# Kernel optimization log

Measured on AMD Instinct MI355X. Metric: run time of the kernel, lower is better.

Reference implementation:

```python
import jax, jax.numpy as jnp
import numpy as np

H, D = 4, 32          # heads, per-head dim (= hidden_channels)
HD = H * D            # concat width fed between layers
L = 2                 # num HGT layers
OUT = 128             # final output dim
SCALE = 1.0 / np.sqrt(D)


def _seg_softmax(score, seg, n):
    # segment softmax over incoming edges per destination node, per head
    mx = jax.ops.segment_max(score, seg, num_segments=n)
    ex = jnp.exp(score - mx[seg])
    den = jax.ops.segment_sum(ex, seg, num_segments=n)
    return ex / den[seg]


def _hgt_side(q_dst, k_src, v_src, src, dst, a_rel, m_rel, p_rel, n_dst):
    # k/v: [N_src,H,D]; a_rel,m_rel: [H,D,D]; p_rel: [H]
    k_t = jnp.einsum('ehd,hdf->ehf', k_src[src], a_rel)          # [E,H,D]
    score = (q_dst[dst] * k_t).sum(-1) * p_rel * SCALE           # [E,H]
    alpha = _seg_softmax(score, dst, n_dst)                      # [E,H]
    v_t = jnp.einsum('ehd,hdf->ehf', v_src[src], m_rel)          # [E,H,D]
    return jax.ops.segment_sum(alpha[..., None] * v_t, dst, num_segments=n_dst)


def _forward(x_m, x_g, W_in_m, b_in_m, W_in_g, b_in_g,
             Wk_m, bk_m, Wq_m, bq_m, Wv_m, bv_m,
             Wk_g, bk_g, Wq_g, bq_g, Wv_g, bv_g,
             a_mg, m_mg, p_mg, a_gm, m_gm, p_gm,
             Wa_m, ba_m, Wa_g, ba_g, skip_m, skip_g,
             W_out_m, b_out_m, W_out_g, b_out_g,
             edge_mg_src, edge_mg_dst, edge_gm_src, edge_gm_dst):
    Nm, Ng = x_m.shape[0], x_g.shape[0]
    # per-node-type input projection
    h_m = x_m @ W_in_m + b_in_m                                  # [Nm,HD]
    h_g = x_g @ W_in_g + b_in_g                                  # [Ng,HD]
    for l in range(L):
        k_m = (h_m @ Wk_m[l] + bk_m[l]).reshape(Nm, H, D)
        q_m = (h_m @ Wq_m[l] + bq_m[l]).reshape(Nm, H, D)
        v_m = (h_m @ Wv_m[l] + bv_m[l]).reshape(Nm, H, D)
        k_g = (h_g @ Wk_g[l] + bk_g[l]).reshape(Ng, H, D)
        q_g = (h_g @ Wq_g[l] + bq_g[l]).reshape(Ng, H, D)
        v_g = (h_g @ Wv_g[l] + bv_g[l]).reshape(Ng, H, D)
        agg_g = _hgt_side(q_g, k_m, v_m, edge_mg_src, edge_mg_dst,
                          a_mg[l], m_mg[l], p_mg[l], Ng)         # [Ng,H,D]
        agg_m = _hgt_side(q_m, k_g, v_g, edge_gm_src, edge_gm_dst,
                          a_gm[l], m_gm[l], p_gm[l], Nm)         # [Nm,H,D]
        o_m = jax.nn.gelu(agg_m.reshape(Nm, HD), approximate=False) @ Wa_m[l] + ba_m[l]
        o_g = jax.nn.gelu(agg_g.reshape(Ng, HD), approximate=False) @ Wa_g[l] + ba_g[l]
        bm = jax.nn.sigmoid(skip_m[l])
        bg = jax.nn.sigmoid(skip_g[l])
        h_m = jax.nn.elu(bm * o_m + (1.0 - bm) * h_m)            # HGTConv skip, then model-level ELU
        h_g = jax.nn.elu(bg * o_g + (1.0 - bg) * h_g)
    out_m = h_m @ W_out_m + b_out_m                              # [Nm,OUT]
    out_g = h_g @ W_out_g + b_out_g                              # [Ng,OUT]
    return jnp.concatenate([out_m, out_g], axis=0)               # [Nm+Ng,OUT]


def setup_inputs() -> dict:
    key = jax.random.key(0)
    ks = iter(jax.random.split(key, 64))
    Nm, Ng, E = 100000, 20000, 500000
    Fm, Fg = 20, 50
    def n(shape, s=0.05):
        return jax.random.normal(next(ks), shape, jnp.float32) * s
    inp = {
        'x_m': n((Nm, Fm), 1.0), 'x_g': n((Ng, Fg), 1.0),
        'W_in_m': n((Fm, HD)), 'b_in_m': jnp.zeros((HD,), jnp.float32),
        'W_in_g': n((Fg, HD)), 'b_in_g': jnp.zeros((HD,), jnp.float32),
        'Wk_m': n((L, HD, HD)), 'bk_m': jnp.zeros((L, HD), jnp.float32),
        'Wq_m': n((L, HD, HD)), 'bq_m': jnp.zeros((L, HD), jnp.float32),
        'Wv_m': n((L, HD, HD)), 'bv_m': jnp.zeros((L, HD), jnp.float32),
        'Wk_g': n((L, HD, HD)), 'bk_g': jnp.zeros((L, HD), jnp.float32),
        'Wq_g': n((L, HD, HD)), 'bq_g': jnp.zeros((L, HD), jnp.float32),
        'Wv_g': n((L, HD, HD)), 'bv_g': jnp.zeros((L, HD), jnp.float32),
        'a_mg': n((L, H, D, D)), 'm_mg': n((L, H, D, D)),
        'p_mg': jnp.ones((L, H), jnp.float32),
        'a_gm': n((L, H, D, D)), 'm_gm': n((L, H, D, D)),
        'p_gm': jnp.ones((L, H), jnp.float32),
        'Wa_m': n((L, HD, HD)), 'ba_m': jnp.zeros((L, HD), jnp.float32),
        'Wa_g': n((L, HD, HD)), 'ba_g': jnp.zeros((L, HD), jnp.float32),
        'skip_m': jnp.ones((L,), jnp.float32), 'skip_g': jnp.ones((L,), jnp.float32),
        'W_out_m': n((HD, OUT)), 'b_out_m': jnp.zeros((OUT,), jnp.float32),
        'W_out_g': n((HD, OUT)), 'b_out_g': jnp.zeros((OUT,), jnp.float32),
        'edge_mg_src': jax.random.randint(next(ks), (E,), 0, Nm, jnp.int32),
        'edge_mg_dst': jax.random.randint(next(ks), (E,), 0, Ng, jnp.int32),
        'edge_gm_src': jax.random.randint(next(ks), (E,), 0, Ng, jnp.int32),
        'edge_gm_dst': jax.random.randint(next(ks), (E,), 0, Nm, jnp.int32),
    }
    return inp


def reference(x_m, x_g, W_in_m, b_in_m, W_in_g, b_in_g,
              Wk_m, bk_m, Wq_m, bq_m, Wv_m, bv_m,
              Wk_g, bk_g, Wq_g, bq_g, Wv_g, bv_g,
              a_mg, m_mg, p_mg, a_gm, m_gm, p_gm,
              Wa_m, ba_m, Wa_g, ba_g, skip_m, skip_g,
              W_out_m, b_out_m, W_out_g, b_out_g,
              edge_mg_src, edge_mg_dst, edge_gm_src, edge_gm_dst):
    return _forward(x_m, x_g, W_in_m, b_in_m, W_in_g, b_in_g,
                    Wk_m, bk_m, Wq_m, bq_m, Wv_m, bv_m,
                    Wk_g, bk_g, Wq_g, bq_g, Wv_g, bv_g,
                    a_mg, m_mg, p_mg, a_gm, m_gm, p_gm,
                    Wa_m, ba_m, Wa_g, ba_g, skip_m, skip_g,
                    W_out_m, b_out_m, W_out_g, b_out_g,
                    edge_mg_src, edge_mg_dst, edge_gm_src, edge_gm_dst)
```

## Files before the change

kernel.cpp:

```cpp
#include <hip/hip_runtime.h>
#include <hip/hip_bf16.h>

#define SCALE_F 0.17677669529663688f

typedef __attribute__((ext_vector_type(8)))  short bfrag;
typedef __attribute__((ext_vector_type(16))) float facc;

__device__ __forceinline__ float lo16(unsigned u){ return __uint_as_float(u << 16); }
__device__ __forceinline__ float hi16(unsigned u){ return __uint_as_float(u & 0xffff0000u); }
__device__ __forceinline__ float bu2f(unsigned short u){ return __uint_as_float((unsigned)u << 16); }
__device__ __forceinline__ unsigned short f2bu(float f){
    __hip_bfloat16 h = __float2bfloat16(f);
    return *reinterpret_cast<unsigned short*>(&h);
}
__device__ __forceinline__ void storeC(float* p, float v){ *p = v; }
__device__ __forceinline__ void storeC(__hip_bfloat16* p, float v){ *p = __float2bfloat16(v); }
__device__ __forceinline__ void up8(uint4 v, float* f){
    f[0]=lo16(v.x); f[1]=hi16(v.x); f[2]=lo16(v.y); f[3]=hi16(v.y);
    f[4]=lo16(v.z); f[5]=hi16(v.z); f[6]=lo16(v.w); f[7]=hi16(v.w);
}

__global__ void hist2_k(const int* __restrict__ d1, int* __restrict__ c1, int E1, int N1,
                        const int* __restrict__ d2, int* __restrict__ c2, int E2, int N2){
    const int* d = blockIdx.y ? d2 : d1;
    int* c = blockIdx.y ? c2 : c1;
    int E = blockIdx.y ? E2 : E1;
    int Nd = blockIdx.y ? N2 : N1;
    int e = blockIdx.x*256 + threadIdx.x;
    if (e >= E) return;
    int dd = d[e];
    if ((unsigned)dd < (unsigned)Nd) atomicAdd(&c[dd], 1);
}

__global__ void scan_block2_k(const int* __restrict__ c1, int* __restrict__ i1, int* __restrict__ b1, int N1,
                              const int* __restrict__ c2, int* __restrict__ i2, int* __restrict__ b2, int N2){
    const int* cnt = blockIdx.y ? c2 : c1;
    int* incl = blockIdx.y ? i2 : i1;
    int* bsum = blockIdx.y ? b2 : b1;
    int N = blockIdx.y ? N2 : N1;
    if ((int)blockIdx.x*256 >= N) return;
    __shared__ int sh[256];
    int tid = threadIdx.x;
    int i = blockIdx.x*256 + tid;
    int v = (i < N) ? cnt[i] : 0;
    sh[tid] = v;
    __syncthreads();
    for (int off = 1; off < 256; off <<= 1){
        int t = (tid >= off) ? sh[tid-off] : 0;
        __syncthreads();
        sh[tid] += t;
        __syncthreads();
    }
    if (i < N) incl[i] = sh[tid];
    if (tid == 255) bsum[blockIdx.x] = sh[255];
}

__global__ void scan_top2_k(int* __restrict__ b1, int nb1, int* __restrict__ b2, int nb2){
    int* bsum = blockIdx.x ? b2 : b1;
    int nb = blockIdx.x ? nb2 : nb1;
    __shared__ int sh[512];
    int tid = threadIdx.x;
    int v = (tid < nb) ? bsum[tid] : 0;
    sh[tid] = v;
    __syncthreads();
    for (int off = 1; off < 512; off <<= 1){
        int t = (tid >= off) ? sh[tid-off] : 0;
        __syncthreads();
        sh[tid] += t;
        __syncthreads();
    }
    if (tid < nb) bsum[tid] = sh[tid] - v;
}

__global__ void finalize2_k(const int* __restrict__ i1, const int* __restrict__ c1,
                            const int* __restrict__ b1, int* __restrict__ p1, int N1, int E1,
                            const int* __restrict__ i2, const int* __restrict__ c2,
                            const int* __restrict__ b2, int* __restrict__ p2, int N2, int E2){
    const int* incl = blockIdx.y ? i2 : i1;
    const int* cnt  = blockIdx.y ? c2 : c1;
    const int* boff = blockIdx.y ? b2 : b1;
    int* indptr = blockIdx.y ? p2 : p1;
    int N = blockIdx.y ? N2 : N1;
    int E = blockIdx.y ? E2 : E1;
    int i = blockIdx.x*256 + threadIdx.x;
    if (i > N) return;
    if (i == N){ indptr[N] = E; return; }
    indptr[i] = boff[i >> 8] + incl[i] - cnt[i];
}

__global__ void scatter2_k(const int* __restrict__ s1, const int* __restrict__ d1,
                           const int* __restrict__ p1, int* __restrict__ u1,
                           int* __restrict__ r1, int E1, int N1,
                           const int* __restrict__ s2, const int* __restrict__ d2,
                           const int* __restrict__ p2, int* __restrict__ u2,
                           int* __restrict__ r2, int E2, int N2){
    const int* src = blockIdx.y ? s2 : s1;
    const int* dst = blockIdx.y ? d2 : d1;
    const int* indptr = blockIdx.y ? p2 : p1;
    int* cur = blockIdx.y ? u2 : u1;
    int* csr = blockIdx.y ? r2 : r1;
    int E = blockIdx.y ? E2 : E1;
    int Nd = blockIdx.y ? N2 : N1;
    int e = blockIdx.x*256 + threadIdx.x;
    if (e >= E) return;
    int d = dst[e];
    if ((unsigned)d >= (unsigned)Nd) return;
    int p = indptr[d] + atomicAdd(&cur[d], 1);
    csr[p] = src[e];
}

template<int K>
__global__ __launch_bounds__(128) void in_proj_k(const float* __restrict__ x,
                                                 const float* __restrict__ W,
                                                 const float* __restrict__ b,
                                                 unsigned short* __restrict__ h, int N){
    constexpr int KP4 = (K + 3)/4, KP = KP4*4;
    int j = threadIdx.x;
    float wreg[KP];
    #pragma unroll
    for (int k = 0; k < KP; ++k) wreg[k] = (k < K) ? W[k*128 + j] : 0.f;
    float bj = b[j];
    __shared__ float xs[8][KP];
    for (int base = blockIdx.x*8; base < N; base += gridDim.x*8){
        __syncthreads();
        for (int t = threadIdx.x; t < 8*KP; t += 128){
            int r = t / KP, k = t - r*KP;
            int row = base + r;
            xs[r][k] = (row < N && k < K) ? x[(size_t)row*K + k] : 0.f;
        }
        __syncthreads();
        #pragma unroll
        for (int r = 0; r < 8; ++r){
            int row = base + r;
            if (row >= N) break;
            float acc = bj;
            #pragma unroll
            for (int kk = 0; kk < KP4; ++kk){
                float4 xv = *(const float4*)(&xs[r][kk*4]);
                acc += xv.x*wreg[kk*4] + xv.y*wreg[kk*4+1]
                     + xv.z*wreg[kk*4+2] + xv.w*wreg[kk*4+3];
            }
            h[(size_t)row*128 + j] = f2bu(acc);
        }
    }
}

__global__ __launch_bounds__(128) void build_wf2_k(
    const float* __restrict__ Wq0, const float* __restrict__ bq0,
    const float* __restrict__ Wk0, const float* __restrict__ bk0,
    const float* __restrict__ Wv0, const float* __restrict__ bv0,
    const float* __restrict__ ar0, const float* __restrict__ mr0,
    unsigned short* __restrict__ Wto0, float* __restrict__ bfo0,
    const float* __restrict__ Wq1, const float* __restrict__ bq1,
    const float* __restrict__ Wk1, const float* __restrict__ bk1,
    const float* __restrict__ Wv1, const float* __restrict__ bv1,
    const float* __restrict__ ar1, const float* __restrict__ mr1,
    unsigned short* __restrict__ Wto1, float* __restrict__ bfo1){
    bool sA = (blockIdx.y == 0);
    const float* Wq = sA ? Wq0 : Wq1;  const float* bq = sA ? bq0 : bq1;
    const float* Wk = sA ? Wk0 : Wk1;  const float* bk = sA ? bk0 : bk1;
    const float* Wv = sA ? Wv0 : Wv1;  const float* bvp = sA ? bv0 : bv1;
    const float* ar = sA ? ar0 : ar1;  const float* mr = sA ? mr0 : mr1;
    unsigned short* Wt = sA ? Wto0 : Wto1;
    float* bf = sA ? bfo0 : bfo1;
    int j = blockIdx.x, row = threadIdx.x;
    int part = j >> 7, f = j & 127, hh = f >> 5, ff = f & 31;
    float v;
    if (part == 0) v = Wq[row*128 + f];
    else {
        const float* Wx  = (part == 1) ? Wk : Wv;
        const float* rel = (part == 1) ? ar : mr;
        float s = 0.f;
        #pragma unroll
        for (int d = 0; d < 32; ++d)
            s += Wx[row*128 + hh*32 + d] * rel[hh*1024 + d*32 + ff];
        v = s;
    }
    Wt[(size_t)j*128 + row] = f2bu(v);
    if (row == 0){
        float bb;
        if (part == 0) bb = bq[f];
        else {
            const float* bx  = (part == 1) ? bk : bvp;
            const float* rel = (part == 1) ? ar : mr;
            float s = 0.f;
            for (int d = 0; d < 32; ++d)
                s += bx[hh*32 + d] * rel[hh*1024 + d*32 + ff];
            bb = s;
        }
        bf[j] = bb;
    }
}

__global__ void transpose6_k(const float* a0, const float* a1, const float* a2,
                             const float* a3, const float* a4, const float* a5,
                             unsigned short* d0, unsigned short* d1, unsigned short* d2,
                             unsigned short* d3, unsigned short* d4, unsigned short* d5){
    int y = blockIdx.y;
    const float* S = (y==0)?a0:(y==1)?a1:(y==2)?a2:(y==3)?a3:(y==4)?a4:a5;
    unsigned short* D = (y==0)?d0:(y==1)?d1:(y==2)?d2:(y==3)?d3:(y==4)?d4:d5;
    int idx = blockIdx.x*256 + threadIdx.x;
    int n = idx >> 7, k = idx & 127;
    D[idx] = f2bu(S[k*128 + n]);
}

template<typename CT, int MODE>
__global__ __launch_bounds__(256) void mfma_gemm2(
    const unsigned short* __restrict__ A0, const unsigned short* __restrict__ Wt0,
    const float* __restrict__ bias0, CT* __restrict__ C0, unsigned short* __restrict__ H0,
    int N0, const float* __restrict__ skip0,
    const unsigned short* __restrict__ A1, const unsigned short* __restrict__ Wt1,
    const float* __restrict__ bias1, CT* __restrict__ C1, unsigned short* __restrict__ H1,
    int N1, const float* __restrict__ skip1,
    int ldc, int nblk0){
    bool s0 = ((int)blockIdx.x < nblk0);
    const unsigned short* A  = s0 ? A0 : A1;
    const unsigned short* Wt = s0 ? Wt0 : Wt1;
    const float* bias = s0 ? bias0 : bias1;
    CT* C = s0 ? C0 : C1;
    unsigned short* H = s0 ? H0 : H1;
    int N = s0 ? N0 : N1;
    const float* skip = s0 ? skip0 : skip1;
    int bx = s0 ? blockIdx.x : (blockIdx.x - nblk0);

    __shared__ unsigned short As[64][136];
    __shared__ unsigned short Bs[128][136];
    int tid = threadIdx.x;
    int rb = bx*64, cb = blockIdx.y*128;
    #pragma unroll
    for (int ph = 0; ph < 4; ++ph){
        int c = ph*256 + tid;
        int r = c >> 4, off = (c & 15)*8;
        uint4 v = make_uint4(0,0,0,0);
        if (rb + r < N) v = ((const uint4*)(A + (size_t)(rb + r)*128))[c & 15];
        *(uint4*)(&As[r][off]) = v;
    }
    #pragma unroll
    for (int ph = 0; ph < 8; ++ph){
        int c = ph*256 + tid;
        int r = c >> 4, off = (c & 15)*8;
        uint4 v = ((const uint4*)(Wt + (size_t)(cb + r)*128))[c & 15];
        *(uint4*)(&Bs[r][off]) = v;
    }
    __syncthreads();
    int w = tid >> 6, lane = tid & 63;
    int wr = (w >> 1)*32, wc = (w & 1)*64;
    int m = lane & 31, quad = lane >> 5;
    facc acc0, acc1;
    #pragma unroll
    for (int i = 0; i < 16; ++i){ acc0[i] = 0.f; acc1[i] = 0.f; }
    const unsigned short* ap  = &As[wr + m][quad*8];
    const unsigned short* bp0 = &Bs[wc + m][quad*8];
    const unsigned short* bp1 = &Bs[wc + 32 + m][quad*8];
    #pragma unroll
    for (int kc = 0; kc < 8; ++kc){
        bfrag a  = *(const bfrag*)(ap  + kc*16);
        bfrag b0 = *(const bfrag*)(bp0 + kc*16);
        bfrag b1 = *(const bfrag*)(bp1 + kc*16);
        acc0 = __builtin_amdgcn_mfma_f32_32x32x16_bf16(a, b0, acc0, 0, 0, 0);
        acc1 = __builtin_amdgcn_mfma_f32_32x32x16_bf16(a, b1, acc1, 0, 0, 0);
    }
    int col0 = cb + wc + m, col1 = col0 + 32;
    float bias0v = bias[col0], bias1v = bias[col1];
    float bm = 0.f;
    if (MODE == 2) bm = 1.f/(1.f + __expf(-skip[0]));
    #pragma unroll
    for (int r = 0; r < 16; ++r){
        int lrow = wr + 4*quad + (r & 3) + 8*(r >> 2);
        int grow = rb + lrow;
        if (grow >= N) continue;
        float o0 = acc0[r] + bias0v;
        float o1 = acc1[r] + bias1v;
        if (MODE == 0){
            storeC(&C[(size_t)grow*ldc + col0], o0);
            storeC(&C[(size_t)grow*ldc + col1], o1);
        } else {
            size_t i0 = (size_t)grow*128 + col0, i1 = (size_t)grow*128 + col1;
            float v0 = bm*o0 + (1.f - bm)*bu2f(H[i0]);
            float v1 = bm*o1 + (1.f - bm)*bu2f(H[i1]);
            v0 = (v0 > 0.f) ? v0 : expm1f(v0);
            v1 = (v1 > 0.f) ? v1 : expm1f(v1);
            H[i0] = f2bu(v0);
            H[i1] = f2bu(v1);
        }
    }
}

__global__ __launch_bounds__(256) void edge_attn4_k(
    const int* __restrict__ ipA, const int* __restrict__ csrA,
    const unsigned short* __restrict__ qdA, const unsigned short* __restrict__ qsA,
    const float* __restrict__ pA, unsigned* __restrict__ aggA, int NdA,
    const int* __restrict__ ipB, const int* __restrict__ csrB,
    const unsigned short* __restrict__ qdB, const unsigned short* __restrict__ qsB,
    const float* __restrict__ pB, unsigned* __restrict__ aggB, int NdB,
    int nblkA){
    bool sA = ((int)blockIdx.x < nblkA);
    const int* ip  = sA ? ipA : ipB;
    const int* csr = sA ? csrA : csrB;
    const unsigned* qd = (const unsigned*)(sA ? qdA : qdB);
    const unsigned* qs = (const unsigned*)(sA ? qsA : qsB);
    const float* p = sA ? pA : pB;
    unsigned* agg = sA ? aggA : aggB;
    int Nd = sA ? NdA : NdB;
    int bx = sA ? blockIdx.x : (blockIdx.x - nblkA);
    int wid  = (bx << 2) | (threadIdx.x >> 6);
    int lane = threadIdx.x & 63;
    if (wid >= Nd) return;
    int slot = lane >> 4, j = lane & 15;
    float ph = p[j >> 2] * SCALE_F;
    uint4 qv = ((const uint4*)(qd + (size_t)wid*192))[j];
    float q[8]; up8(qv, q);
    int beg = ip[wid], end = ip[wid + 1];
    float den = 0.f;
    float acc[8] = {0.f,0.f,0.f,0.f,0.f,0.f,0.f,0.f};
    int i = beg + slot;
    if (i < end){
        int s = csr[i];
        const uint4* b = (const uint4*)(qs + (size_t)s*192);
        uint4 kv = b[16 + j];
        uint4 vv = b[32 + j];
        while (true){
            int inx = i + 4;
            bool more = (inx < end);
            uint4 kv2, vv2;
            if (more){
                int s2 = csr[inx];
                const uint4* b2 = (const uint4*)(qs + (size_t)s2*192);
                kv2 = b2[16 + j];
                vv2 = b2[32 + j];
            }
            float kf[8]; up8(kv, kf);
            float part = q[0]*kf[0] + q[1]*kf[1] + q[2]*kf[2] + q[3]*kf[3]
                       + q[4]*kf[4] + q[5]*kf[5] + q[6]*kf[6] + q[7]*kf[7];
            part += __shfl_xor(part, 1);
            part += __shfl_xor(part, 2);
            float e = __expf(part * ph);
            float vf[8]; up8(vv, vf);
            den += e;
            #pragma unroll
            for (int d = 0; d < 8; ++d) acc[d] += e * vf[d];
            if (!more) break;
            i = inx; kv = kv2; vv = vv2;
        }
    }
    den += __shfl_xor(den, 16);
    den += __shfl_xor(den, 32);
    #pragma unroll
    for (int d = 0; d < 8; ++d){
        acc[d] += __shfl_xor(acc[d], 16);
        acc[d] += __shfl_xor(acc[d], 32);
    }
    float inv = (den > 0.f) ? 1.f/den : 0.f;
    float o0 = acc[2*slot]*inv, o1 = acc[2*slot + 1]*inv;
    o0 = 0.5f*o0*(1.f + erff(o0*0.70710678118654752f));
    o1 = 0.5f*o1*(1.f + erff(o1*0.70710678118654752f));
    agg[(size_t)wid*64 + j*4 + slot] = (unsigned)f2bu(o0) | ((unsigned)f2bu(o1) << 16);
}

extern "C" void kernel_launch(void* const* d_in, const int* in_sizes, int n_in,
                              void* d_out, int out_size, void* d_ws, size_t ws_size,
                              hipStream_t stream){
    typedef const float* FP;
    FP x_m = (FP)d_in[0], x_g = (FP)d_in[1];
    FP W_in_m = (FP)d_in[2], b_in_m = (FP)d_in[3], W_in_g = (FP)d_in[4], b_in_g = (FP)d_in[5];
    FP Wk_m = (FP)d_in[6],  bk_m = (FP)d_in[7],  Wq_m = (FP)d_in[8],  bq_m = (FP)d_in[9];
    FP Wv_m = (FP)d_in[10], bv_m = (FP)d_in[11];
    FP Wk_g = (FP)d_in[12], bk_g = (FP)d_in[13], Wq_g = (FP)d_in[14], bq_g = (FP)d_in[15];
    FP Wv_g = (FP)d_in[16], bv_g = (FP)d_in[17];
    FP a_mg = (FP)d_in[18], m_mg = (FP)d_in[19], p_mg = (FP)d_in[20];
    FP a_gm = (FP)d_in[21], m_gm = (FP)d_in[22], p_gm = (FP)d_in[23];
    FP Wa_m = (FP)d_in[24], ba_m = (FP)d_in[25], Wa_g = (FP)d_in[26], ba_g = (FP)d_in[27];
    FP skip_m = (FP)d_in[28], skip_g = (FP)d_in[29];
    FP W_out_m = (FP)d_in[30], b_out_m = (FP)d_in[31], W_out_g = (FP)d_in[32], b_out_g = (FP)d_in[33];
    const int* e_mg_src = (const int*)d_in[34];
    const int* e_mg_dst = (const int*)d_in[35];
    const int* e_gm_src = (const int*)d_in[36];
    const int* e_gm_dst = (const int*)d_in[37];

    const int Nm = in_sizes[0] / 20;
    const int Ng = in_sizes[1] / 50;
    const int E1 = in_sizes[34];
    const int E2 = in_sizes[36];

    char* wp = (char*)d_ws;
    auto alloc = [&](size_t bytes) -> char* {
        char* r = wp; wp += (bytes + 255) & ~(size_t)255; return r;
    };
    unsigned short* h_m   = (unsigned short*)alloc((size_t)Nm*128*2);
    unsigned short* h_g   = (unsigned short*)alloc((size_t)Ng*128*2);
    unsigned short* agg_m = (unsigned short*)alloc((size_t)Nm*128*2);
    unsigned short* agg_g = (unsigned short*)alloc((size_t)Ng*128*2);
    unsigned short* qkv_m = (unsigned short*)alloc((size_t)Nm*384*2);
    unsigned short* qkv_g = (unsigned short*)alloc((size_t)Ng*384*2);
    unsigned short* Wtf   = (unsigned short*)alloc((size_t)4*49152*2);
    float*          bfv   = (float*)alloc((size_t)4*384*4);
    unsigned short* Wta   = (unsigned short*)alloc((size_t)4*16384*2);
    unsigned short* Wtout = (unsigned short*)alloc((size_t)2*16384*2);
    int* indptr_g = (int*)alloc((size_t)(Ng+1)*4);
    int* csr_mg   = (int*)alloc((size_t)E1*4);
    int* indptr_m = (int*)alloc((size_t)(Nm+1)*4);
    int* csr_gm   = (int*)alloc((size_t)E2*4);
    int maxN = Nm > Ng ? Nm : Ng;
    int* cnt  = (int*)alloc((size_t)maxN*4);
    int* cur  = (int*)alloc((size_t)maxN*4);
    int* cnt2 = (int*)alloc((size_t)maxN*4);
    int* cur2 = (int*)alloc((size_t)maxN*4);
    int* incl = (int*)alloc((size_t)maxN*4);
    int* incl2= (int*)alloc((size_t)maxN*4);
    int* bsum = (int*)alloc(512*4);
    int* bsum2= (int*)alloc(512*4);

    size_t used = (size_t)(wp - (char*)d_ws);
    if (used > ws_size){
        hipMemsetAsync(d_out, 0, (size_t)out_size*4, stream);
        return;
    }
    hipMemsetAsync(cnt, 0, (size_t)((char*)cur2 - (char*)cnt) + (size_t)maxN*4, stream);

    int maxE = E1 > E2 ? E1 : E2;
    int nb1 = (Ng + 255)/256, nb2 = (Nm + 255)/256;
    int nbmax = nb1 > nb2 ? nb1 : nb2;
    hist2_k<<<dim3((maxE + 255)/256, 2), 256, 0, stream>>>(
        e_mg_dst, cnt, E1, Ng, e_gm_dst, cnt2, E2, Nm);
    scan_block2_k<<<dim3(nbmax, 2), 256, 0, stream>>>(
        cnt, incl, bsum, Ng, cnt2, incl2, bsum2, Nm);
    scan_top2_k<<<2, 512, 0, stream>>>(bsum, nb1, bsum2, nb2);
    finalize2_k<<<dim3(nbmax + 1, 2), 256, 0, stream>>>(
        incl, cnt, bsum, indptr_g, Ng, E1, incl2, cnt2, bsum2, indptr_m, Nm, E2);
    scatter2_k<<<dim3((maxE + 255)/256, 2), 256, 0, stream>>>(
        e_mg_src, e_mg_dst, indptr_g, cur, csr_mg, E1, Ng,
        e_gm_src, e_gm_dst, indptr_m, cur2, csr_gm, E2, Nm);

    transpose6_k<<<dim3(64, 6), 256, 0, stream>>>(
        Wa_m, Wa_g, Wa_m + 16384, Wa_g + 16384, W_out_m, W_out_g,
        Wta, Wta + 16384, Wta + 32768, Wta + 49152, Wtout, Wtout + 16384);
    for (int l = 0; l < 2; ++l){
        build_wf2_k<<<dim3(384, 2), 128, 0, stream>>>(
            Wq_m + l*16384, bq_m + l*128, Wk_m + l*16384, bk_m + l*128,
            Wv_m + l*16384, bv_m + l*128, a_mg + l*4096, m_mg + l*4096,
            Wtf + (size_t)(l*2+0)*49152, bfv + (l*2+0)*384,
            Wq_g + l*16384, bq_g + l*128, Wk_g + l*16384, bk_g + l*128,
            Wv_g + l*16384, bv_g + l*128, a_gm + l*4096, m_gm + l*4096,
            Wtf + (size_t)(l*2+1)*49152, bfv + (l*2+1)*384);
    }

    int gim = (Nm + 7)/8; if (gim > 2048) gim = 2048;
    int gig = (Ng + 7)/8; if (gig > 2048) gig = 2048;
    in_proj_k<20><<<gim, 128, 0, stream>>>(x_m, W_in_m, b_in_m, h_m, Nm);
    in_proj_k<50><<<gig, 128, 0, stream>>>(x_g, W_in_g, b_in_g, h_g, Ng);

    int gxm = (Nm + 63)/64, gxg = (Ng + 63)/64;
    int nbA = (Ng + 3)/4, nbB = (Nm + 3)/4;

    for (int l = 0; l < 2; ++l){
        mfma_gemm2<__hip_bfloat16, 0><<<dim3(gxm + gxg, 3), 256, 0, stream>>>(
            h_m, Wtf + (size_t)(l*2+0)*49152, bfv + (l*2+0)*384,
            (__hip_bfloat16*)qkv_m, nullptr, Nm, nullptr,
            h_g, Wtf + (size_t)(l*2+1)*49152, bfv + (l*2+1)*384,
            (__hip_bfloat16*)qkv_g, nullptr, Ng, nullptr,
            384, gxm);

        edge_attn4_k<<<nbA + nbB, 256, 0, stream>>>(
            indptr_g, csr_mg, qkv_g, qkv_m, p_mg + l*4, (unsigned*)agg_g, Ng,
            indptr_m, csr_gm, qkv_m, qkv_g, p_gm + l*4, (unsigned*)agg_m, Nm,
            nbA);

        mfma_gemm2<float, 2><<<dim3(gxm + gxg, 1), 256, 0, stream>>>(
            agg_m, Wta + (size_t)(l*2+0)*16384, ba_m + l*128, (float*)nullptr, h_m, Nm, skip_m + l,
            agg_g, Wta + (size_t)(l*2+1)*16384, ba_g + l*128, (float*)nullptr, h_g, Ng, skip_g + l,
            128, gxm);
    }

    float* outp = (float*)d_out;
    mfma_gemm2<float, 0><<<dim3(gxm + gxg, 1), 256, 0, stream>>>(
        h_m, Wtout, b_out_m, outp, nullptr, Nm, nullptr,
        h_g, Wtout + 16384, b_out_g, outp + (size_t)Nm*128, nullptr, Ng, nullptr,
        128, gxm);
}
```

Measured before the change: 621.0 us.

## Reuse A tile across QKV column chunks; deepen edge-attention prefetch with packed math

The QKV GEMM now loops over the three 128-column chunks inside one block, so each A tile is loaded into shared memory once instead of once per grid-y block. The cost is a third as many blocks and serialized weight loads. The edge attention kernel prefetches the CSR index two edges ahead, uses packed float2 arithmetic, and replaces __expf with native exp2 using a pre-scaled log2e factor. Together these aim to cut redundant global loads and shorten the gather and latency chain in the edge loop.

```diff
diff --git a/kernel.cpp b/kernel.cpp
--- a/kernel.cpp
+++ b/kernel.cpp
@@ -5,6 +5,9 @@
 
 typedef __attribute__((ext_vector_type(8)))  short bfrag;
 typedef __attribute__((ext_vector_type(16))) float facc;
+typedef __attribute__((ext_vector_type(2)))  float f32x2;
+
+extern "C" __device__ float __ocml_native_exp2_f32(float);
 
 __device__ __forceinline__ float lo16(unsigned u){ return __uint_as_float(u << 16); }
 __device__ __forceinline__ float hi16(unsigned u){ return __uint_as_float(u & 0xffff0000u); }
@@ -15,10 +18,6 @@
 }
 __device__ __forceinline__ void storeC(float* p, float v){ *p = v; }
 __device__ __forceinline__ void storeC(__hip_bfloat16* p, float v){ *p = __float2bfloat16(v); }
-__device__ __forceinline__ void up8(uint4 v, float* f){
-    f[0]=lo16(v.x); f[1]=hi16(v.x); f[2]=lo16(v.y); f[3]=hi16(v.y);
-    f[4]=lo16(v.z); f[5]=hi16(v.z); f[6]=lo16(v.w); f[7]=hi16(v.w);
-}
 
 __global__ void hist2_k(const int* __restrict__ d1, int* __restrict__ c1, int E1, int N1,
                         const int* __restrict__ d2, int* __restrict__ c2, int E2, int N2){
@@ -204,7 +203,7 @@
     D[idx] = f2bu(S[k*128 + n]);
 }
 
-template<typename CT, int MODE>
+template<typename CT, int MODE, int NCHUNK>
 __global__ __launch_bounds__(256) void mfma_gemm2(
     const unsigned short* __restrict__ A0, const unsigned short* __restrict__ Wt0,
     const float* __restrict__ bias0, CT* __restrict__ C0, unsigned short* __restrict__ H0,
@@ -226,7 +225,7 @@
     __shared__ unsigned short As[64][136];
     __shared__ unsigned short Bs[128][136];
     int tid = threadIdx.x;
-    int rb = bx*64, cb = blockIdx.y*128;
+    int rb = bx*64;
     #pragma unroll
     for (int ph = 0; ph < 4; ++ph){
         int c = ph*256 + tid;
@@ -235,58 +234,63 @@
         if (rb + r < N) v = ((const uint4*)(A + (size_t)(rb + r)*128))[c & 15];
         *(uint4*)(&As[r][off]) = v;
     }
-    #pragma unroll
-    for (int ph = 0; ph < 8; ++ph){
-        int c = ph*256 + tid;
-        int r = c >> 4, off = (c & 15)*8;
-        uint4 v = ((const uint4*)(Wt + (size_t)(cb + r)*128))[c & 15];
-        *(uint4*)(&Bs[r][off]) = v;
-    }
-    __syncthreads();
     int w = tid >> 6, lane = tid & 63;
     int wr = (w >> 1)*32, wc = (w & 1)*64;
     int m = lane & 31, quad = lane >> 5;
-    facc acc0, acc1;
-    #pragma unroll
-    for (int i = 0; i < 16; ++i){ acc0[i] = 0.f; acc1[i] = 0.f; }
     const unsigned short* ap  = &As[wr + m][quad*8];
     const unsigned short* bp0 = &Bs[wc + m][quad*8];
     const unsigned short* bp1 = &Bs[wc + 32 + m][quad*8];
-    #pragma unroll
-    for (int kc = 0; kc < 8; ++kc){
-        bfrag a  = *(const bfrag*)(ap  + kc*16);
-        bfrag b0 = *(const bfrag*)(bp0 + kc*16);
-        bfrag b1 = *(const bfrag*)(bp1 + kc*16);
-        acc0 = __builtin_amdgcn_mfma_f32_32x32x16_bf16(a, b0, acc0, 0, 0, 0);
-        acc1 = __builtin_amdgcn_mfma_f32_32x32x16_bf16(a, b1, acc1, 0, 0, 0);
-    }
-    int col0 = cb + wc + m, col1 = col0 + 32;
-    float bias0v = bias[col0], bias1v = bias[col1];
     float bm = 0.f;
     if (MODE == 2) bm = 1.f/(1.f + __expf(-skip[0]));
-    #pragma unroll
-    for (int r = 0; r < 16; ++r){
-        int lrow = wr + 4*quad + (r & 3) + 8*(r >> 2);
-        int grow = rb + lrow;
-        if (grow >= N) continue;
-        float o0 = acc0[r] + bias0v;
-        float o1 = acc1[r] + bias1v;
-        if (MODE == 0){
-            storeC(&C[(size_t)grow*ldc + col0], o0);
-            storeC(&C[(size_t)grow*ldc + col1], o1);
-        } else {
-            size_t i0 = (size_t)grow*128 + col0, i1 = (size_t)grow*128 + col1;
-            float v0 = bm*o0 + (1.f - bm)*bu2f(H[i0]);
-            float v1 = bm*o1 + (1.f - bm)*bu2f(H[i1]);
-            v0 = (v0 > 0.f) ? v0 : expm1f(v0);
-            v1 = (v1 > 0.f) ? v1 : expm1f(v1);
-            H[i0] = f2bu(v0);
-            H[i1] = f2bu(v1);
-        }
-    }
-}
-
-__global__ __launch_bounds__(256) void edge_attn4_k(
+
+    for (int chunk = 0; chunk < NCHUNK; ++chunk){
+        int cb = (NCHUNK == 1) ? (int)blockIdx.y*128 : chunk*128;
+        if (chunk > 0) __syncthreads();
+        #pragma unroll
+        for (int ph = 0; ph < 8; ++ph){
+            int c = ph*256 + tid;
+            int r = c >> 4, off = (c & 15)*8;
+            uint4 v = ((const uint4*)(Wt + (size_t)(cb + r)*128))[c & 15];
+            *(uint4*)(&Bs[r][off]) = v;
+        }
+        __syncthreads();
+        facc acc0, acc1;
+        #pragma unroll
+        for (int i = 0; i < 16; ++i){ acc0[i] = 0.f; acc1[i] = 0.f; }
+        #pragma unroll
+        for (int kc = 0; kc < 8; ++kc){
+            bfrag a  = *(const bfrag*)(ap  + kc*16);
+            bfrag b0 = *(const bfrag*)(bp0 + kc*16);
+            bfrag b1 = *(const bfrag*)(bp1 + kc*16);
+            acc0 = __builtin_amdgcn_mfma_f32_32x32x16_bf16(a, b0, acc0, 0, 0, 0);
+            acc1 = __builtin_amdgcn_mfma_f32_32x32x16_bf16(a, b1, acc1, 0, 0, 0);
+        }
+        int col0 = cb + wc + m, col1 = col0 + 32;
+        float bias0v = bias[col0], bias1v = bias[col1];
+        #pragma unroll
+        for (int r = 0; r < 16; ++r){
+            int lrow = wr + 4*quad + (r & 3) + 8*(r >> 2);
+            int grow = rb + lrow;
+            if (grow >= N) continue;
+            float o0 = acc0[r] + bias0v;
+            float o1 = acc1[r] + bias1v;
+            if (MODE == 0){
+                storeC(&C[(size_t)grow*ldc + col0], o0);
+                storeC(&C[(size_t)grow*ldc + col1], o1);
+            } else {
+                size_t i0 = (size_t)grow*128 + col0, i1 = (size_t)grow*128 + col1;
+                float v0 = bm*o0 + (1.f - bm)*bu2f(H[i0]);
+                float v1 = bm*o1 + (1.f - bm)*bu2f(H[i1]);
+                v0 = (v0 > 0.f) ? v0 : expm1f(v0);
+                v1 = (v1 > 0.f) ? v1 : expm1f(v1);
+                H[i0] = f2bu(v0);
+                H[i1] = f2bu(v1);
+            }
+        }
+    }
+}
+
+__global__ __launch_bounds__(256) void edge_attn5_k(
     const int* __restrict__ ipA, const int* __restrict__ csrA,
     const unsigned short* __restrict__ qdA, const unsigned short* __restrict__ qsA,
     const float* __restrict__ pA, unsigned* __restrict__ aggA, int NdA,
@@ -298,7 +302,7 @@
     const int* ip  = sA ? ipA : ipB;
     const int* csr = sA ? csrA : csrB;
     const unsigned* qd = (const unsigned*)(sA ? qdA : qdB);
-    const unsigned* qs = (const unsigned*)(sA ? qsA : qsB);
+    const char* qsc = (const char*)(sA ? qsA : qsB);
     const float* p = sA ? pA : pB;
     unsigned* agg = sA ? aggA : aggB;
     int Nd = sA ? NdA : NdB;
@@ -307,51 +311,70 @@
     int lane = threadIdx.x & 63;
     if (wid >= Nd) return;
     int slot = lane >> 4, j = lane & 15;
-    float ph = p[j >> 2] * SCALE_F;
+    float phL = p[j >> 2] * (SCALE_F * 1.4426950408889634f);
     uint4 qv = ((const uint4*)(qd + (size_t)wid*192))[j];
-    float q[8]; up8(qv, q);
+    f32x2 q2[4];
+    q2[0] = (f32x2){lo16(qv.x), hi16(qv.x)};
+    q2[1] = (f32x2){lo16(qv.y), hi16(qv.y)};
+    q2[2] = (f32x2){lo16(qv.z), hi16(qv.z)};
+    q2[3] = (f32x2){lo16(qv.w), hi16(qv.w)};
     int beg = ip[wid], end = ip[wid + 1];
     float den = 0.f;
-    float acc[8] = {0.f,0.f,0.f,0.f,0.f,0.f,0.f,0.f};
-    int i = beg + slot;
-    if (i < end){
-        int s = csr[i];
-        const uint4* b = (const uint4*)(qs + (size_t)s*192);
-        uint4 kv = b[16 + j];
-        uint4 vv = b[32 + j];
+    f32x2 acc2[4] = {};
+    int loff = j*16;
+    int i0 = beg + slot;
+    if (i0 < end){
+        int s0c = csr[i0];
+        int i1 = i0 + 4;
+        bool m1 = (i1 < end);
+        int s1 = m1 ? csr[i1] : 0;
+        const char* b0 = qsc + (size_t)s0c*768 + loff;
+        uint4 kv = *(const uint4*)(b0 + 256);
+        uint4 vv = *(const uint4*)(b0 + 512);
         while (true){
-            int inx = i + 4;
-            bool more = (inx < end);
+            int i2 = i1 + 4;
+            bool m2 = (i2 < end);
+            int s2 = m2 ? csr[i2] : 0;
             uint4 kv2, vv2;
-            if (more){
-                int s2 = csr[inx];
-                const uint4* b2 = (const uint4*)(qs + (size_t)s2*192);
-                kv2 = b2[16 + j];
-                vv2 = b2[32 + j];
+            if (m1){
+                const char* b1 = qsc + (size_t)s1*768 + loff;
+                kv2 = *(const uint4*)(b1 + 256);
+                vv2 = *(const uint4*)(b1 + 512);
             }
-            float kf[8]; up8(kv, kf);
-            float part = q[0]*kf[0] + q[1]*kf[1] + q[2]*kf[2] + q[3]*kf[3]
-                       + q[4]*kf[4] + q[5]*kf[5] + q[6]*kf[6] + q[7]*kf[7];
+            f32x2 pp = q2[0] * (f32x2){lo16(kv.x), hi16(kv.x)};
+            pp += q2[1] * (f32x2){lo16(kv.y), hi16(kv.y)};
+            pp += q2[2] * (f32x2){lo16(kv.z), hi16(kv.z)};
+            pp += q2[3] * (f32x2){lo16(kv.w), hi16(kv.w)};
+            float part = pp.x + pp.y;
             part += __shfl_xor(part, 1);
             part += __shfl_xor(part, 2);
-            float e = __expf(part * ph);
-            float vf[8]; up8(vv, vf);
+            float e = __ocml_native_exp2_f32(part * phL);
             den += e;
-            #pragma unroll
-            for (int d = 0; d < 8; ++d) acc[d] += e * vf[d];
-            if (!more) break;
-            i = inx; kv = kv2; vv = vv2;
+            acc2[0] += (f32x2){lo16(vv.x), hi16(vv.x)} * e;
+            acc2[1] += (f32x2){lo16(vv.y), hi16(vv.y)} * e;
+            acc2[2] += (f32x2){lo16(vv.z), hi16(vv.z)} * e;
+            acc2[3] += (f32x2){lo16(vv.w), hi16(vv.w)} * e;
+            if (!m1) break;
+            kv = kv2; vv = vv2;
+            i1 = i2; m1 = m2; s1 = s2;
         }
     }
     den += __shfl_xor(den, 16);
     den += __shfl_xor(den, 32);
     #pragma unroll
-    for (int d = 0; d < 8; ++d){
-        acc[d] += __shfl_xor(acc[d], 16);
-        acc[d] += __shfl_xor(acc[d], 32);
+    for (int k = 0; k < 4; ++k){
+        f32x2 t;
+        t.x = __shfl_xor(acc2[k].x, 16);
+        t.y = __shfl_xor(acc2[k].y, 16);
+        acc2[k] += t;
+        t.x = __shfl_xor(acc2[k].x, 32);
+        t.y = __shfl_xor(acc2[k].y, 32);
+        acc2[k] += t;
     }
     float inv = (den > 0.f) ? 1.f/den : 0.f;
-    float o0 = acc[2*slot]*inv, o1 = acc[2*slot + 1]*inv;
+    f32x2 sel = (slot & 2) ? ((slot & 1) ? acc2[3] : acc2[2])
+                           : ((slot & 1) ? acc2[1] : acc2[0]);
+    float o0 = sel.x*inv, o1 = sel.y*inv;
     o0 = 0.5f*o0*(1.f + erff(o0*0.70710678118654752f));
     o1 = 0.5f*o1*(1.f + erff(o1*0.70710678118654752f));
     agg[(size_t)wid*64 + j*4 + slot] = (unsigned)f2bu(o0) | ((unsigned)f2bu(o1) << 16);
@@ -453,26 +476,26 @@
     int nbA = (Ng + 3)/4, nbB = (Nm + 3)/4;
 
     for (int l = 0; l < 2; ++l){
-        mfma_gemm2<__hip_bfloat16, 0><<<dim3(gxm + gxg, 3), 256, 0, stream>>>(
+        mfma_gemm2<__hip_bfloat16, 0, 3><<<dim3(gxm + gxg, 1), 256, 0, stream>>>(
             h_m, Wtf + (size_t)(l*2+0)*49152, bfv + (l*2+0)*384,
             (__hip_bfloat16*)qkv_m, nullptr, Nm, nullptr,
             h_g, Wtf + (size_t)(l*2+1)*49152, bfv + (l*2+1)*384,
             (__hip_bfloat16*)qkv_g, nullptr, Ng, nullptr,
             384, gxm);
 
-        edge_attn4_k<<<nbA + nbB, 256, 0, stream>>>(
+        edge_attn5_k<<<nbA + nbB, 256, 0, stream>>>(
             indptr_g, csr_mg, qkv_g, qkv_m, p_mg + l*4, (unsigned*)agg_g, Ng,
             indptr_m, csr_gm, qkv_m, qkv_g, p_gm + l*4, (unsigned*)agg_m, Nm,
             nbA);
 
-        mfma_gemm2<float, 2><<<dim3(gxm + gxg, 1), 256, 0, stream>>>(
+        mfma_gemm2<float, 2, 1><<<dim3(gxm + gxg, 1), 256, 0, stream>>>(
             agg_m, Wta + (size_t)(l*2+0)*16384, ba_m + l*128, (float*)nullptr, h_m, Nm, skip_m + l,
             agg_g, Wta + (size_t)(l*2+1)*16384, ba_g + l*128, (float*)nullptr, h_g, Ng, skip_g + l,
             128, gxm);
     }
 
     float* outp = (float*)d_out;
-    mfma_gemm2<float, 0><<<dim3(gxm + gxg, 1), 256, 0, stream>>>(
+    mfma_gemm2<float, 0, 1><<<dim3(gxm + gxg, 1), 256, 0, stream>>>(
         h_m, Wtout, b_out_m, outp, nullptr, Nm, nullptr,
         h_g, Wtout + 16384, b_out_g, outp + (size_t)Nm*128, nullptr, Ng, nullptr,
         128, gxm);
```

Result: no change. 614.4 us (-1.1%).
